# Kernel optimization log

Measured on AMD Instinct MI355X. Metric: run time of the kernel, lower is better.

The kernel has to match this reference:

```python
import jax, jax.numpy as jnp
import numpy as np

KS = 5               # kernel_size per spline dimension
K3 = KS ** 3         # 125 weight matrices per SplineConv
NS = [16384, 4096, 1024, 256, 64]  # nodes per hierarchy level
DEG = 8


def spline_basis(pseudo):
    """Degree-1 open B-spline basis for 3D pseudo-coords in [0,1].
    Returns basis [E,8] and weight indices [E,8] into the K3 weights."""
    v = pseudo * (KS - 1)
    bot = jnp.minimum(jnp.floor(v), KS - 2)
    frac = v - bot                                  # [E,3]
    bot = bot.astype(jnp.int32)
    bits = jnp.array([[(s >> d) & 1 for d in range(3)] for s in range(8)], jnp.int32)  # [8,3]
    f = frac[:, None, :]                            # [E,1,3]
    basis = jnp.prod(jnp.where(bits[None] == 1, f, 1.0 - f), axis=-1)   # [E,8]
    strides = jnp.array([1, KS, KS * KS], jnp.int32)
    widx = jnp.sum((bot[:, None, :] + bits[None]) * strides, axis=-1)   # [E,8]
    return basis, widx


def spline_conv(x, src, dst, basis, widx, W, root, bias, n):
    """out_j = (1/deg_j) * sum_{i->j} sum_s B_s(u_ij) x_i W_{k(s)} + x_j root + bias.
    Accumulate basis-weighted source features into per-(node, weight-index)
    buckets, then one dense einsum with the 125 kernel weights."""
    in_c = x.shape[1]
    contrib = basis[..., None] * x[src][:, None, :]          # [E,8,in]
    flat = (dst[:, None] * K3 + widx).reshape(-1)            # [E*8]
    acc = jnp.zeros((n * K3, in_c), x.dtype).at[flat].add(contrib.reshape(-1, in_c))
    out = jnp.einsum('nki,kio->no', acc.reshape(n, K3, in_c), W)
    deg = jnp.zeros((n,), x.dtype).at[dst].add(1.0)
    return out / jnp.maximum(deg, 1.0)[:, None] + x @ root + bias


def setup_inputs() -> dict:
    rng = np.random.default_rng(0)
    inp = {}
    inp['x'] = jnp.asarray(rng.standard_normal((NS[0], 1)), jnp.float32)
    for l in range(4):
        e = NS[l] * DEG
        inp[f'src{l}'] = jnp.asarray(rng.integers(0, NS[l], e), jnp.int32)
        inp[f'dst{l}'] = jnp.asarray(rng.integers(0, NS[l], e), jnp.int32)
        inp[f'pseudo{l}'] = jnp.asarray(rng.random((e, 3)), jnp.float32)
        cl = np.arange(NS[l]) % NS[l + 1]  # guarantees every voxel cluster non-empty
        rng.shuffle(cl)
        inp[f'cluster{l}'] = jnp.asarray(cl, jnp.int32)
    chans = [(1, 32), (32, 32), (32, 64), (64, 64), (64, 64), (64, 64), (64, 64), (64, 64)]
    names = ['1', '12', '2', '3', '4', '5', '6', '7']
    for nm, (ci, co) in zip(names, chans):
        inp[f'W{nm}'] = jnp.asarray(rng.standard_normal((K3, ci, co)) / np.sqrt(8.0 * ci), jnp.float32)
        inp[f'R{nm}'] = jnp.asarray(rng.standard_normal((ci, co)) / np.sqrt(ci), jnp.float32)
        inp[f'B{nm}'] = jnp.zeros((co,), jnp.float32)
    inp['fc1_w'] = jnp.asarray(rng.standard_normal((64, 64)) / 8.0, jnp.float32)
    inp['fc1_b'] = jnp.zeros((64,), jnp.float32)
    inp['fc2_w'] = jnp.asarray(rng.standard_normal((64, 10)) / 8.0, jnp.float32)
    inp['fc2_b'] = jnp.zeros((10,), jnp.float32)
    return inp


def reference(x, pseudo0, pseudo1, pseudo2, pseudo3,
              src0, dst0, src1, dst1, src2, dst2, src3, dst3,
              cluster0, cluster1, cluster2, cluster3,
              W1, R1, B1, W12, R12, B12, W2, R2, B2, W3, R3, B3,
              W4, R4, B4, W5, R5, B5, W6, R6, B6, W7, R7, B7,
              fc1_w, fc1_b, fc2_w, fc2_b):
    elu = jax.nn.elu
    # level 0
    b, wi = spline_basis(pseudo0)
    h = elu(spline_conv(x, src0, dst0, b, wi, W1, R1, B1, NS[0]))
    h = elu(spline_conv(h, src0, dst0, b, wi, W12, R12, B12, NS[0]))
    h = jax.ops.segment_max(h, cluster0, num_segments=NS[1])   # voxel max pool 1
    # level 1
    b, wi = spline_basis(pseudo1)
    h = elu(spline_conv(h, src1, dst1, b, wi, W2, R2, B2, NS[1]))
    h = elu(spline_conv(h, src1, dst1, b, wi, W3, R3, B3, NS[1]))
    h = jax.ops.segment_max(h, cluster1, num_segments=NS[2])   # voxel max pool 2
    # level 2
    b, wi = spline_basis(pseudo2)
    h = elu(spline_conv(h, src2, dst2, b, wi, W4, R4, B4, NS[2]))
    h = elu(spline_conv(h, src2, dst2, b, wi, W5, R5, B5, NS[2]))
    h = jax.ops.segment_max(h, cluster2, num_segments=NS[3])   # voxel max pool 3
    # level 3
    b, wi = spline_basis(pseudo3)
    h = elu(spline_conv(h, src3, dst3, b, wi, W6, R6, B6, NS[3]))
    h = elu(spline_conv(h, src3, dst3, b, wi, W7, R7, B7, NS[3]))
    h = jax.ops.segment_max(h, cluster3, num_segments=NS[4])   # voxel max pool 4
    # readout head (dropout is identity in eval mode)
    g = h.mean(0)[None, :]
    g = g @ fc1_w + fc1_b
    g = g @ fc2_w + fc2_b
    return jax.nn.log_softmax(g, axis=1)
```

## Files before the change

kernel.cpp:

```cpp
#include <hip/hip_runtime.h>
#include <hip/hip_bf16.h>

#define KS 5
#define K3 125

typedef __attribute__((ext_vector_type(8))) short short8;
typedef __attribute__((ext_vector_type(4))) float floatx4;

__device__ inline unsigned enc_f(float f) {
    int b = __float_as_int(f);
    return (b >= 0) ? ((unsigned)b | 0x80000000u) : ~((unsigned)b);
}

__device__ inline unsigned short f2bf(float f) {
    unsigned u = __float_as_uint(f);
    u += 0x7FFFu + ((u >> 16) & 1u);
    return (unsigned short)(u >> 16);
}
__device__ inline float bf2f(unsigned short h) {
    return __uint_as_float((unsigned)h << 16);
}
__device__ inline unsigned pack2bf(float a, float b) {
    return (unsigned)f2bf(a) | ((unsigned)f2bf(b) << 16);
}

__device__ inline void edge_basis(const float* __restrict__ pseudo, int e,
                                  float* bs, int* ks) {
    float fr[3];
    int bot[3];
#pragma unroll
    for (int d = 0; d < 3; ++d) {
        float v = pseudo[e * 3 + d] * (float)(KS - 1);
        float fl = fminf(floorf(v), (float)(KS - 2));
        fr[d] = v - fl;
        bot[d] = (int)fl;
    }
    const int strides[3] = {1, KS, KS * KS};
#pragma unroll
    for (int s = 0; s < 8; ++s) {
        float b = 1.f;
        int w = 0;
#pragma unroll
        for (int d = 0; d < 3; ++d) {
            int bit = (s >> d) & 1;
            b *= bit ? fr[d] : (1.f - fr[d]);
            w += (bot[d] + bit) * strides[d];
        }
        bs[s] = b;
        ks[s] = w;
    }
}

__device__ inline void edge_fracs(const float* __restrict__ pseudo, int e, float* bs) {
    float fr[3];
#pragma unroll
    for (int d = 0; d < 3; ++d) {
        float v = pseudo[e * 3 + d] * (float)(KS - 1);
        float fl = fminf(floorf(v), (float)(KS - 2));
        fr[d] = v - fl;
    }
#pragma unroll
    for (int s = 0; s < 8; ++s) {
        float b = 1.f;
#pragma unroll
        for (int d = 0; d < 3; ++d) b *= ((s >> d) & 1) ? fr[d] : (1.f - fr[d]);
        bs[s] = b;
    }
}

__device__ inline int edge_bucket(const float* __restrict__ pseudo, int e) {
    int kb = 0;
#pragma unroll
    for (int d = 0; d < 3; ++d) {
        float v = pseudo[e * 3 + d] * (float)(KS - 1);
        int fl = (int)fminf(floorf(v), (float)(KS - 2));
        kb += fl << (2 * d);
    }
    return kb;
}

__global__ __launch_bounds__(256) void pre1(
    const float* __restrict__ p0, const float* __restrict__ p1,
    const float* __restrict__ p2, const float* __restrict__ p3,
    const int* __restrict__ d0, const int* __restrict__ d1,
    const int* __restrict__ d2, const int* __restrict__ d3,
    const int* __restrict__ c0, const int* __restrict__ c1,
    const int* __restrict__ c2, const int* __restrict__ c3,
    const float* __restrict__ w12, const float* __restrict__ w2,
    const float* __restrict__ w3, const float* __restrict__ w4,
    const float* __restrict__ w5, const float* __restrict__ w6,
    const float* __restrict__ w7,
    int* __restrict__ hpart, int* __restrict__ degi,
    int* __restrict__ ccnt, int* __restrict__ clist,
    short* __restrict__ Wt) {
    __shared__ float wls[64 * 65];
    __shared__ int h[64];
    int b = blockIdx.x;
    int t = threadIdx.x;
    if (b >= 765) {
        int sl = b - 765;
        const float* srcp;
        int IC, OC, lgI, lgO, per;
        size_t obase;
        if (sl < 125) {
            IC = 32; OC = 32; lgI = 5; lgO = 5; per = 1024;
            srcp = w12 + (size_t)sl * 1024;
            obase = (size_t)sl * 1024;
        } else if (sl < 250) {
            int k = sl - 125;
            IC = 32; OC = 64; lgI = 5; lgO = 6; per = 2048;
            srcp = w2 + (size_t)k * 2048;
            obase = 128000 + (size_t)k * 2048;
        } else {
            int q = sl - 250;
            int ts = q / 125;
            int k = q - ts * 125;
            const float* Ws[5] = {w3, w4, w5, w6, w7};
            IC = 64; OC = 64; lgI = 6; lgO = 6; per = 4096;
            srcp = Ws[ts] + (size_t)k * 4096;
            obase = 384000 + (size_t)ts * 512000 + (size_t)k * 4096;
        }
        for (int r = t; r < per; r += 256) {
            int i = r >> lgO, o = r & (OC - 1);
            wls[i * (OC + 1) + o] = srcp[r];
        }
        __syncthreads();
        for (int j = t; j < per; j += 256) {
            int o = j >> lgI, i = j & (IC - 1);
            Wt[obase + j] = (short)f2bf(wls[i * (OC + 1) + o]);
        }
        return;
    }
    if (b >= 680) {
        int idx = (b - 680) * 256 + t;
        int j, cof, nof;
        const int* cl;
        if (idx < 16384)      { j = idx;         cl = c0; cof = 0;    nof = 0; }
        else if (idx < 20480) { j = idx - 16384; cl = c1; cof = 4096; nof = 16384; }
        else if (idx < 21504) { j = idx - 20480; cl = c2; cof = 5120; nof = 20480; }
        else if (idx < 21760) { j = idx - 21504; cl = c3; cof = 5376; nof = 21504; }
        else return;
        int c = cl[j];
        int slot = atomicAdd(&ccnt[cof + c], 1) & 3;
        clist[nof + c * 4 + slot] = j;
        return;
    }
    int l, lb, E, dof;
    const float* ps;
    const int* ds;
    if (b < 512)      { l = 0; lb = b;       ps = p0; ds = d0; E = 131072; dof = 0; }
    else if (b < 640) { l = 1; lb = b - 512; ps = p1; ds = d1; E = 32768;  dof = 16384; }
    else if (b < 672) { l = 2; lb = b - 640; ps = p2; ds = d2; E = 8192;   dof = 20480; }
    else              { l = 3; lb = b - 672; ps = p3; ds = d3; E = 2048;   dof = 21504; }
    if (t < 64) h[t] = 0;
    __syncthreads();
    int e = lb * 256 + t;
    if (e < E) {
        atomicAdd(&h[edge_bucket(ps, e)], 1);
        atomicAdd(&degi[dof + ds[e]], 1);
    }
    __syncthreads();
    if (t < 64) hpart[b * 64 + t] = h[t];
}

__global__ __launch_bounds__(1024) void pre2(const int* __restrict__ hpart,
                                             int* __restrict__ bbase,
                                             int* __restrict__ tileOf,
                                             int* __restrict__ pack,
                                             const int* __restrict__ degi,
                                             int* __restrict__ off,
                                             int* __restrict__ cur) {
    int b = blockIdx.x;
    int t = threadIdx.x;
    __shared__ int ls[1024];
    __shared__ int aux[192];
    if (b < 4) {
        const int Nv[4] = {16384, 4096, 1024, 256};
        const int DOFv[4] = {0, 16384, 20480, 21504};
        const int OFFv[4] = {0, 16385, 20482, 21507};
        int l = b;
        int n = Nv[l];
        const int* d = degi + DOFv[l];
        int* o = off + OFFv[l];
        int* c = cur + DOFv[l];
        int per = (n + 1023) >> 10;
        int beg = t * per;
        int end = (beg + per < n) ? beg + per : n;
        int s = 0;
        for (int j = beg; j < end; ++j) s += d[j];
        ls[t] = s;
        __syncthreads();
        for (int dd = 1; dd < 1024; dd <<= 1) {
            int v = (t >= dd) ? ls[t - dd] : 0;
            __syncthreads();
            ls[t] += v;
            __syncthreads();
        }
        int base = (t == 0) ? 0 : ls[t - 1];
        for (int j = beg; j < end; ++j) {
            o[j] = base;
            c[j] = base;
            base += d[j];
        }
        if (t == 1023) o[n] = ls[1023];
    } else {
        const int TBv[4] = {0, 2112, 2688, 2880};
        const int MTv[4] = {2112, 576, 192, 96};
        const int HBv[4] = {0, 512, 640, 672};
        const int NBv[4] = {512, 128, 32, 8};
        int l = b - 4;
        int tileBase = TBv[l];
        int hb = HBv[l], nb = NBv[l];
        int bucket = t & 63, seg = t >> 6;
        int rps = (nb + 15) >> 4;
        int r0 = seg * rps;
        int r1 = r0 + rps;
        if (r1 > nb) r1 = nb;
        int ssum = 0;
        for (int lb = r0; lb < r1; ++lb) ssum += hpart[(hb + lb) * 64 + bucket];
        ls[seg * 64 + bucket] = ssum;
        __syncthreads();
        int pre = 0;
        for (int s2 = 0; s2 < seg; ++s2) pre += ls[s2 * 64 + bucket];
        if (seg == 15) aux[bucket] = pre + ssum;
        __syncthreads();
        if (t < 64) aux[64 + t] = (aux[t] + 63) >> 6;
        __syncthreads();
        for (int d = 1; d < 64; d <<= 1) {
            int v = 0;
            if (t < 64 && t >= d) v = aux[64 + t - d];
            __syncthreads();
            if (t < 64) aux[64 + t] += v;
            __syncthreads();
        }
        if (t < 64) {
            int cnt = aux[t];
            int tiles = (cnt + 63) >> 6;
            int tb = tileBase + aux[64 + t] - tiles;
            int gstart = tb * 64;
            aux[128 + t] = gstart;
            for (int q = 0; q < tiles; ++q) tileOf[tb + q] = t;
            for (int idx = gstart + cnt; idx < (tb + tiles) * 64; ++idx) pack[idx] = -1;
            if (t == 63) {
                for (int q = tileBase + aux[64 + 63]; q < tileBase + MTv[l]; ++q)
                    tileOf[q] = -1;
            }
        }
        __syncthreads();
        int run = aux[128 + bucket] + pre;
        for (int lb = r0; lb < r1; ++lb) {
            bbase[(hb + lb) * 64 + bucket] = run;
            run += hpart[(hb + lb) * 64 + bucket];
        }
    }
}

__global__ __launch_bounds__(256) void scatter_pos_all(
    const float* __restrict__ p0, const float* __restrict__ p1,
    const float* __restrict__ p2, const float* __restrict__ p3,
    const int* __restrict__ d0, const int* __restrict__ d1,
    const int* __restrict__ d2, const int* __restrict__ d3,
    const int* __restrict__ bbase, int* __restrict__ cur,
    int* __restrict__ pack, int* __restrict__ posArr,
    int* __restrict__ esrt) {
    int b = blockIdx.x;
    int l, lb, E, dof, eof_;
    const float* ps;
    const int* ds;
    if (b < 512)      { l = 0; lb = b;       ps = p0; ds = d0; E = 131072; dof = 0;     eof_ = 0; }
    else if (b < 640) { l = 1; lb = b - 512; ps = p1; ds = d1; E = 32768;  dof = 16384; eof_ = 131072; }
    else if (b < 672) { l = 2; lb = b - 640; ps = p2; ds = d2; E = 8192;   dof = 20480; eof_ = 163840; }
    else              { l = 3; lb = b - 672; ps = p3; ds = d3; E = 2048;   dof = 21504; eof_ = 172032; }
    __shared__ int h[64], lbk[64], gb[64], sh[64];
    __shared__ int sp[256];
    __shared__ unsigned char skk[256];
    int t = threadIdx.x;
    int e = lb * 256 + t;
    int kb = -1;
    if (t < 64) {
        h[t] = 0;
        gb[t] = bbase[b * 64 + t];
    }
    __syncthreads();
    if (e < E) {
        kb = edge_bucket(ps, e);
        atomicAdd(&h[kb], 1);
        int p = atomicAdd(&cur[dof + ds[e]], 1);
        posArr[eof_ + e] = p;
        if (l == 0 && p >= 0 && p < 131072) esrt[p] = e;
    }
    __syncthreads();
    if (t < 64) sh[t] = h[t];
    __syncthreads();
    for (int d = 1; d < 64; d <<= 1) {
        int v = (t < 64 && t >= d) ? sh[t - d] : 0;
        __syncthreads();
        if (t < 64) sh[t] += v;
        __syncthreads();
    }
    if (t < 64) {
        lbk[t] = sh[t] - h[t];
        h[t] = 0;
    }
    __syncthreads();
    if (kb >= 0) {
        int ppos = lbk[kb] + atomicAdd(&h[kb], 1);
        sp[ppos] = e;
        skk[ppos] = (unsigned char)kb;
    }
    __syncthreads();
    int Pb = E - lb * 256;
    if (Pb > 256) Pb = 256;
    if (t < Pb) {
        int k = skk[t];
        pack[gb[k] + (t - lbk[k])] = sp[t];
    }
}

__global__ __launch_bounds__(256) void conv1_fin(
    const float* __restrict__ x, const int* __restrict__ src,
    const float* __restrict__ pseudo, const int* __restrict__ esrt,
    const int* __restrict__ off, const float* __restrict__ W,
    const float* __restrict__ R, const float* __restrict__ B,
    float* __restrict__ out, int n, int Emax) {
    const int lane = threadIdx.x & 63;
    const int wid = threadIdx.x >> 6;
    const int sub = lane >> 5;
    const int o = lane & 31;
    int j = (blockIdx.x * 4 + wid) * 2 + sub;
    if (j >= n) return;
    int b0 = off[j], b1 = off[j + 1];
    if (b0 < 0) b0 = 0;
    if (b1 > Emax) b1 = Emax;
    float acc = 0.f;
    for (int r = b0; r < b1; ++r) {
        int e = esrt[r];
        float bs[8];
        int ks[8];
        edge_basis(pseudo, e, bs, ks);
        float w = 0.f;
#pragma unroll
        for (int s = 0; s < 8; ++s) w = fmaf(bs[s], W[ks[s] * 32 + o], w);
        acc = fmaf(w, x[src[e]], acc);
    }
    float d = fmaxf((float)(b1 - b0), 1.f);
    float v = acc / d + x[j] * R[o] + B[o];
    out[(size_t)j * 32 + o] = (v > 0.f) ? v : expm1f(v);
}

template <int IN_C, int OUT_C>
__global__ __launch_bounds__(256, 6) void mfma_conv(
    const float* __restrict__ x, const int* __restrict__ src,
    const float* __restrict__ pseudo, const int* __restrict__ pack,
    const int* __restrict__ tileOf, const int* __restrict__ pos,
    const short* __restrict__ Wt, unsigned short* __restrict__ y, int tileBase,
    int Emax) {
    constexpr int PH = (IN_C == 64) ? 4 : 2;
    constexpr int SPP = 8 / PH;
    constexpr int KPH = SPP * IN_C;
    constexpr int KP = KPH + 8;
    constexpr int NT = OUT_C / 16;
    constexpr int IP = IN_C / 4;
    __shared__ short As[64 * KP];
    __shared__ int posL[64];
    const int tid = threadIdx.x;
    int t = tileBase + blockIdx.x;
    int kb = tileOf[t];
    if (kb < 0 || kb >= 64) return;
    kb = __builtin_amdgcn_readfirstlane(kb);
    const int kbase = (kb & 3) + 5 * ((kb >> 2) & 3) + 25 * ((kb >> 4) & 3);
    const int eLoc = tid >> 2, part = tid & 3;
    int e = pack[t * 64 + eLoc];
    if (e >= Emax) e = -1;
    float bs[8];
    float4 xq[IP / 4];
    if (e >= 0) edge_fracs(pseudo, e, bs);
    else {
#pragma unroll
        for (int s = 0; s < 8; ++s) bs[s] = 0.f;
    }
    if (part == 0) posL[eLoc] = (e >= 0) ? pos[e] : -1;
#pragma unroll
    for (int g = 0; g < IP / 4; ++g)
        xq[g] = (e >= 0)
                    ? *(const float4*)(x + (size_t)src[e] * IN_C + part * IP + g * 4)
                    : make_float4(0.f, 0.f, 0.f, 0.f);
    const int wave = tid >> 6, lane = tid & 63;
    const int quad = lane >> 4, lm = lane & 15;
    floatx4 acc[NT];
#pragma unroll
    for (int nt = 0; nt < NT; ++nt) acc[nt] = (floatx4){0.f, 0.f, 0.f, 0.f};
    const short* myrow = &As[(wave * 16 + lm) * KP];
#pragma unroll
    for (int ph = 0; ph < PH; ++ph) {
        if (ph) __syncthreads();
#pragma unroll
        for (int s2 = 0; s2 < SPP; ++s2) {
            const float b = bs[ph * SPP + s2];
            short* rowp = &As[eLoc * KP + s2 * IN_C + part * IP];
#pragma unroll
            for (int g = 0; g < IP / 4; ++g) {
                unsigned lo = pack2bf(b * xq[g].x, b * xq[g].y);
                unsigned hi = pack2bf(b * xq[g].z, b * xq[g].w);
                *(uint2*)(rowp + 4 * g) = make_uint2(lo, hi);
            }
        }
        __syncthreads();
#pragma unroll
        for (int kstep = 0; kstep < KPH / 32; ++kstep) {
            const int kg = kstep * 32;
            const int s2 = kg / IN_C;
            const int i0 = kg % IN_C;
            const int s = ph * SPP + s2;
            const int ks = kbase + (s & 1) + 5 * ((s >> 1) & 1) + 25 * ((s >> 2) & 1);
            short8 a = *(const short8*)&myrow[kg + quad * 8];
#pragma unroll
            for (int nt = 0; nt < NT; ++nt) {
                const short* bp =
                    Wt + ((size_t)ks * OUT_C + nt * 16 + lm) * IN_C + i0 + quad * 8;
                short8 bfr = *(const short8*)bp;
                acc[nt] = __builtin_amdgcn_mfma_f32_16x16x32_bf16(a, bfr, acc[nt], 0, 0, 0);
            }
        }
    }
#pragma unroll
    for (int nt = 0; nt < NT; ++nt) {
#pragma unroll
        for (int r = 0; r < 4; ++r) {
            int row = wave * 16 + quad * 4 + r;
            int p = posL[row];
            if (p >= 0 && p < Emax) y[(size_t)p * OUT_C + nt * 16 + lm] = f2bf(acc[nt][r]);
        }
    }
}

template <int OUT_C>
__device__ inline float csr_sum(const int* __restrict__ off,
                                const unsigned short* __restrict__ y, int j, int o,
                                float& dcount) {
    int b0 = off[j], b1 = off[j + 1];
    if (b0 < 0) b0 = 0;
    if (b1 < b0) b1 = b0;
    dcount = fmaxf((float)(b1 - b0), 1.f);
    float s0 = 0.f, s1 = 0.f, s2 = 0.f, s3 = 0.f;
    int r = b0;
    for (; r + 4 <= b1; r += 4) {
        s0 += bf2f(y[(size_t)(r + 0) * OUT_C + o]);
        s1 += bf2f(y[(size_t)(r + 1) * OUT_C + o]);
        s2 += bf2f(y[(size_t)(r + 2) * OUT_C + o]);
        s3 += bf2f(y[(size_t)(r + 3) * OUT_C + o]);
    }
    for (; r < b1; ++r) s0 += bf2f(y[(size_t)r * OUT_C + o]);
    return (s0 + s1) + (s2 + s3);
}

template <int IN_C, int OUT_C>
__global__ __launch_bounds__(256) void fin_gather_k(
    const float* __restrict__ xin, const float* __restrict__ R,
    const float* __restrict__ B, const int* __restrict__ off,
    const unsigned short* __restrict__ y, float* __restrict__ out, int n) {
    const int lane = threadIdx.x & 63;
    const int wid = threadIdx.x >> 6;
    constexpr int EPW = 64 / OUT_C;
    const int sub = (EPW == 2) ? (lane >> 5) : 0;
    const int o = lane & (OUT_C - 1);
    int j = (blockIdx.x * (blockDim.x >> 6) + wid) * EPW + sub;
    if (j >= n) return;
    float xv = (o < IN_C) ? xin[j * IN_C + o] : 0.f;
    float acc = B[o];
#pragma unroll 4
    for (int i = 0; i < IN_C; ++i) {
        float xi = __shfl(xv, i, OUT_C);
        acc = fmaf(xi, R[i * OUT_C + o], acc);
    }
    float d;
    float s = csr_sum<OUT_C>(off, y, j, o, d);
    float v = s / d + acc;
    out[j * OUT_C + o] = (v > 0.f) ? v : expm1f(v);
}

template <int IN_C, int OUT_C>
__global__ __launch_bounds__(256) void fin_pool_k(
    const float* __restrict__ xin, const float* __restrict__ R,
    const float* __restrict__ B, const int* __restrict__ off,
    const unsigned short* __restrict__ y, const int* __restrict__ clist,
    float* __restrict__ out, int nsrc) {
    constexpr int CPB = 256 / (4 * OUT_C);
    const int t = threadIdx.x;
    const int o = t & (OUT_C - 1);
    const int mem = (t / OUT_C) & 3;
    const int g = t / (4 * OUT_C);
    const int c = blockIdx.x * CPB + g;
    int j = clist[c * 4 + mem];
    if (j < 0) j = 0;
    if (j >= nsrc) j = nsrc - 1;
    float xv = (o < IN_C) ? xin[(size_t)j * IN_C + o] : 0.f;
    float acc = B[o];
#pragma unroll 4
    for (int i = 0; i < IN_C; ++i) {
        float xi = __shfl(xv, i, OUT_C);
        acc = fmaf(xi, R[i * OUT_C + o], acc);
    }
    float d;
    float s = csr_sum<OUT_C>(off, y, j, o, d);
    float v = s / d + acc;
    v = (v > 0.f) ? v : expm1f(v);
    __shared__ float sh[256];
    sh[t] = v;
    __syncthreads();
    if (mem == 0) {
        const float* base = &sh[g * 4 * OUT_C];
        float r01 = fmaxf(base[o], base[OUT_C + o]);
        float r23 = fmaxf(base[2 * OUT_C + o], base[3 * OUT_C + o]);
        out[(size_t)c * OUT_C + o] = fmaxf(r01, r23);
    }
}

__global__ __launch_bounds__(256) void conv1_fused(const float* __restrict__ x,
                                                   const int* __restrict__ src,
                                                   const int* __restrict__ dst,
                                                   const float* __restrict__ pseudo,
                                                   const float* __restrict__ W,
                                                   float* __restrict__ out, int E) {
    const int lane = threadIdx.x & 63;
    const int wid = threadIdx.x >> 6;
    const int sub = lane >> 5;
    const int o = lane & 31;
    int e = (blockIdx.x * 4 + wid) * 2 + sub;
    if (e >= E) return;
    float bs[8];
    int ks[8];
    edge_basis(pseudo, e, bs, ks);
    float acc = 0.f;
#pragma unroll
    for (int s = 0; s < 8; ++s) acc = fmaf(bs[s], W[ks[s] * 32 + o], acc);
    atomicAdd(&out[(size_t)dst[e] * 32 + o], acc * x[src[e]]);
}

template <int IN_C, int OUT_C>
__global__ __launch_bounds__(256) void conv_edges_inline(
    const float* __restrict__ x, const int* __restrict__ src,
    const int* __restrict__ dst, const float* __restrict__ pseudo,
    const float* __restrict__ W, float* __restrict__ out, int E) {
    const int lane = threadIdx.x & 63;
    const int wid = threadIdx.x >> 6;
    constexpr int EPW = 64 / OUT_C;
    const int sub = (EPW == 2) ? (lane >> 5) : 0;
    const int o = lane & (OUT_C - 1);
    long e = (long)(blockIdx.x * (blockDim.x >> 6) + wid) * EPW + sub;
    if (e >= E) return;
    float bs[8];
    int ks[8];
    edge_basis(pseudo, e, bs, ks);
    const int s_ = src[e];
    const int d_ = dst[e];
    float xv = (o < IN_C) ? x[s_ * IN_C + o] : 0.f;
    float acc = 0.f;
#pragma unroll
    for (int s = 0; s < 8; ++s) {
        const float b = bs[s];
        const float* Wk = W + (long)ks[s] * IN_C * OUT_C;
#pragma unroll 4
        for (int i = 0; i < IN_C; ++i) {
            float xi = __shfl(xv, i, OUT_C);
            acc = fmaf(b * xi, Wk[i * OUT_C + o], acc);
        }
    }
    atomicAdd(&out[(long)d_ * OUT_C + o], acc);
}

__global__ void deg_kernel(const int* __restrict__ dst, float* __restrict__ deg, int E) {
    int e = blockIdx.x * blockDim.x + threadIdx.x;
    if (e >= E) return;
    atomicAdd(&deg[dst[e]], 1.0f);
}

template <int IN_C, int OUT_C>
__global__ __launch_bounds__(256) void finalize_k(
    const float* __restrict__ xin, const float* __restrict__ R,
    const float* __restrict__ B, const float* __restrict__ deg,
    float* __restrict__ out, int n) {
    const int lane = threadIdx.x & 63;
    const int wid = threadIdx.x >> 6;
    constexpr int EPW = 64 / OUT_C;
    const int sub = (EPW == 2) ? (lane >> 5) : 0;
    const int o = lane & (OUT_C - 1);
    int j = (blockIdx.x * (blockDim.x >> 6) + wid) * EPW + sub;
    if (j >= n) return;
    float xv = (o < IN_C) ? xin[j * IN_C + o] : 0.f;
    float acc = B[o];
#pragma unroll 4
    for (int i = 0; i < IN_C; ++i) {
        float xi = __shfl(xv, i, OUT_C);
        acc = fmaf(xi, R[i * OUT_C + o], acc);
    }
    float d = fmaxf(deg[j], 1.f);
    float v = out[j * OUT_C + o] / d + acc;
    out[j * OUT_C + o] = (v > 0.f) ? v : expm1f(v);
}

__global__ void pool_scatter(const float* __restrict__ h, const int* __restrict__ cluster,
                             unsigned* __restrict__ pool, int n, int logC) {
    int idx = blockIdx.x * blockDim.x + threadIdx.x;
    if (idx >= (n << logC)) return;
    int j = idx >> logC;
    int c = idx & ((1 << logC) - 1);
    atomicMax(&pool[(cluster[j] << logC) + c], enc_f(h[idx]));
}

__global__ void pool_decode(const unsigned* __restrict__ pool, float* __restrict__ out, int total) {
    int idx = blockIdx.x * blockDim.x + threadIdx.x;
    if (idx >= total) return;
    unsigned u = pool[idx];
    int b = (u & 0x80000000u) ? (int)(u & 0x7FFFFFFFu) : (int)(~u);
    out[idx] = __int_as_float(b);
}

__global__ void head_kernel(const float* __restrict__ h, const float* __restrict__ fc1w,
                            const float* __restrict__ fc1b, const float* __restrict__ fc2w,
                            const float* __restrict__ fc2b, float* __restrict__ out) {
    __shared__ float m[64], t[64], u[10];
    int lane = threadIdx.x;
    float s = 0.f;
    for (int j = 0; j < 64; ++j) s += h[j * 64 + lane];
    m[lane] = s * (1.f / 64.f);
    __syncthreads();
    float a = fc1b[lane];
    for (int i = 0; i < 64; ++i) a = fmaf(m[i], fc1w[i * 64 + lane], a);
    t[lane] = a;
    __syncthreads();
    if (lane < 10) {
        float b = fc2b[lane];
        for (int i = 0; i < 64; ++i) b = fmaf(t[i], fc2w[i * 10 + lane], b);
        u[lane] = b;
    }
    __syncthreads();
    if (lane < 10) {
        float mx = u[0];
        for (int i = 1; i < 10; ++i) mx = fmaxf(mx, u[i]);
        float se = 0.f;
        for (int i = 0; i < 10; ++i) se += expf(u[i] - mx);
        out[lane] = u[lane] - mx - logf(se);
    }
}

static inline int cdiv(int a, int b) { return (a + b - 1) / b; }

extern "C" void kernel_launch(void* const* d_in, const int* in_sizes, int n_in,
                              void* d_out, int out_size, void* d_ws, size_t ws_size,
                              hipStream_t stream) {
    const float* x = (const float*)d_in[0];
    const int* src[4] = {(const int*)d_in[1], (const int*)d_in[5], (const int*)d_in[9], (const int*)d_in[13]};
    const int* dst[4] = {(const int*)d_in[2], (const int*)d_in[6], (const int*)d_in[10], (const int*)d_in[14]};
    const float* pseudo[4] = {(const float*)d_in[3], (const float*)d_in[7], (const float*)d_in[11], (const float*)d_in[15]};
    const int* cluster[4] = {(const int*)d_in[4], (const int*)d_in[8], (const int*)d_in[12], (const int*)d_in[16]};
    const float* Wp[8], *Rp[8], *Bp[8];
    for (int l = 0; l < 8; ++l) {
        Wp[l] = (const float*)d_in[17 + 3 * l];
        Rp[l] = (const float*)d_in[18 + 3 * l];
        Bp[l] = (const float*)d_in[19 + 3 * l];
    }
    const float* fc1w = (const float*)d_in[41];
    const float* fc1b = (const float*)d_in[42];
    const float* fc2w = (const float*)d_in[43];
    const float* fc2b = (const float*)d_in[44];
    float* outp = (float*)d_out;

    const int NS[5] = {16384, 4096, 1024, 256, 64};
    const int ES[4] = {16384 * 8, 4096 * 8, 1024 * 8, 256 * 8};
    const int MT[4] = {2048 + 64, 512 + 64, 128 + 64, 32 + 64};
    const int TB_[4] = {0, 2112, 2112 + 576, 2112 + 576 + 192};
    const int TOT_TILES = 2112 + 576 + 192 + 96;
    const int DTOT = 21760;
    const int OFF2[4] = {0, 16385, 20482, 21507};
    const int OFFTOT = 21764;
    const int EBASE[4] = {0, 131072, 163840, 172032};
    const int ETOT = 174080;
    const int NODE_OFF[4] = {0, 16384, 20480, 21504};
    const int CCTOT = 4096 + 1024 + 256 + 64;
    const int HTOT = 680;
    const int WT_OFF[7] = {0, 128000, 384000, 896000, 1408000, 1920000, 2432000};
    const int WT_TOT = 2944000;
    const int NSLICE = 875;

    char* w = (char*)d_ws;
    auto take = [&](size_t bytes) -> char* {
        char* r = w;
        w += (bytes + 255) & ~(size_t)255;
        return r;
    };
    float* bufA = (float*)take((size_t)NS[0] * 64 * 4);
    float* bufB = (float*)take((size_t)NS[0] * 64 * 4);
    unsigned* pool = (unsigned*)take((size_t)NS[1] * 64 * 4);
    char* zbase = w;
    int* ccnt = (int*)take((size_t)CCTOT * 4);
    int* degi = (int*)take((size_t)DTOT * 4);
    size_t zbytes = (size_t)(w - zbase);
    size_t fallbackNeed = (size_t)(w - (char*)d_ws);
    int* tileOf = (int*)take((size_t)TOT_TILES * 4);
    int* hpart = (int*)take((size_t)HTOT * 64 * 4);
    int* bbase = (int*)take((size_t)HTOT * 64 * 4);
    int* pack = (int*)take((size_t)TOT_TILES * 64 * 4);
    int* csr = (int*)take((size_t)OFFTOT * 4);
    int* cur = (int*)take((size_t)DTOT * 4);
    int* posArr = (int*)take((size_t)ETOT * 4);
    int* clist = (int*)take((size_t)DTOT * 4);
    int* esrt = (int*)take((size_t)ES[0] * 4);
    short* Wtb = (short*)take((size_t)WT_TOT * 2);
    unsigned short* y = (unsigned short*)take((size_t)ES[0] * 32 * 2);
    size_t need = (size_t)(w - (char*)d_ws);
    bool fast = ws_size >= need;

    const int TB = 256;

    if (fast) {
        (void)hipMemsetAsync(zbase, 0, zbytes, stream);
        pre1<<<765 + NSLICE, 256, 0, stream>>>(
            pseudo[0], pseudo[1], pseudo[2], pseudo[3],
            dst[0], dst[1], dst[2], dst[3],
            cluster[0], cluster[1], cluster[2], cluster[3],
            Wp[1], Wp[2], Wp[3], Wp[4], Wp[5], Wp[6], Wp[7],
            hpart, degi, ccnt, clist, Wtb);
        pre2<<<8, 1024, 0, stream>>>(hpart, bbase, tileOf, pack, degi, csr, cur);
        scatter_pos_all<<<680, 256, 0, stream>>>(pseudo[0], pseudo[1], pseudo[2], pseudo[3],
                                                 dst[0], dst[1], dst[2], dst[3],
                                                 bbase, cur, pack, posArr, esrt);

        {
            int n = NS[0];
            const int* off = csr + OFF2[0];
            const int* pos = posArr + EBASE[0];
            conv1_fin<<<cdiv(n, 8), TB, 0, stream>>>(x, src[0], pseudo[0], esrt, off,
                                                     Wp[0], Rp[0], Bp[0], bufA, n, ES[0]);
            mfma_conv<32, 32><<<MT[0], TB, 0, stream>>>(
                bufA, src[0], pseudo[0], pack, tileOf, pos, Wtb + WT_OFF[0], y, TB_[0], ES[0]);
            fin_pool_k<32, 32><<<NS[1] / 2, TB, 0, stream>>>(
                bufA, Rp[1], Bp[1], off, y, clist + NODE_OFF[0], bufB, NS[0]);
        }
        {
            int n = NS[1];
            const int* off = csr + OFF2[1];
            const int* pos = posArr + EBASE[1];
            mfma_conv<32, 64><<<MT[1], TB, 0, stream>>>(
                bufB, src[1], pseudo[1], pack, tileOf, pos, Wtb + WT_OFF[1], y, TB_[1], ES[1]);
            fin_gather_k<32, 64><<<cdiv(n, 4), TB, 0, stream>>>(bufB, Rp[2], Bp[2], off, y, bufA, n);
            mfma_conv<64, 64><<<MT[1], TB, 0, stream>>>(
                bufA, src[1], pseudo[1], pack, tileOf, pos, Wtb + WT_OFF[2], y, TB_[1], ES[1]);
            fin_pool_k<64, 64><<<NS[2], TB, 0, stream>>>(
                bufA, Rp[3], Bp[3], off, y, clist + NODE_OFF[1], bufB, NS[1]);
        }
        {
            int n = NS[2];
            const int* off = csr + OFF2[2];
            const int* pos = posArr + EBASE[2];
            mfma_conv<64, 64><<<MT[2], TB, 0, stream>>>(
                bufB, src[2], pseudo[2], pack, tileOf, pos, Wtb + WT_OFF[3], y, TB_[2], ES[2]);
            fin_gather_k<64, 64><<<cdiv(n, 4), TB, 0, stream>>>(bufB, Rp[4], Bp[4], off, y, bufA, n);
            mfma_conv<64, 64><<<MT[2], TB, 0, stream>>>(
                bufA, src[2], pseudo[2], pack, tileOf, pos, Wtb + WT_OFF[4], y, TB_[2], ES[2]);
            fin_pool_k<64, 64><<<NS[3], TB, 0, stream>>>(
                bufA, Rp[5], Bp[5], off, y, clist + NODE_OFF[2], bufB, NS[2]);
        }
        {
            int n = NS[3];
            const int* off = csr + OFF2[3];
            const int* pos = posArr + EBASE[3];
            mfma_conv<64, 64><<<MT[3], TB, 0, stream>>>(
                bufB, src[3], pseudo[3], pack, tileOf, pos, Wtb + WT_OFF[5], y, TB_[3], ES[3]);
            fin_gather_k<64, 64><<<cdiv(n, 4), TB, 0, stream>>>(bufB, Rp[6], Bp[6], off, y, bufA, n);
            mfma_conv<64, 64><<<MT[3], TB, 0, stream>>>(
                bufA, src[3], pseudo[3], pack, tileOf, pos, Wtb + WT_OFF[6], y, TB_[3], ES[3]);
            fin_pool_k<64, 64><<<NS[4], TB, 0, stream>>>(
                bufA, Rp[7], Bp[7], off, y, clist + NODE_OFF[3], bufB, NS[3]);
        }
        head_kernel<<<1, 64, 0, stream>>>(bufB, fc1w, fc1b, fc2w, fc2b, outp);
    } else if (ws_size >= fallbackNeed) {
        float* h0 = bufA;
        float* h1 = bufB;
        float* deg = (float*)degi;
        for (int l = 0; l < 4; ++l) {
            int E = ES[l], n = NS[l];
            (void)hipMemsetAsync(deg, 0, n * 4, stream);
            deg_kernel<<<cdiv(E, TB), TB, 0, stream>>>(dst[l], deg, E);
            for (int cc = 0; cc < 2; ++cc) {
                int li = (l == 0) ? cc : 2 * l + cc;
                if (l == 0 && cc == 0) {
                    (void)hipMemsetAsync(h0, 0, (size_t)n * 32 * 4, stream);
                    conv1_fused<<<cdiv(E, 8), TB, 0, stream>>>(x, src[0], dst[0], pseudo[0], Wp[0], h0, E);
                    finalize_k<1, 32><<<cdiv(n, 8), TB, 0, stream>>>(x, Rp[0], Bp[0], deg, h0, n);
                } else {
                    int ic = (l == 0) ? 32 : ((l == 1 && cc == 0) ? 32 : 64);
                    int oc = (l == 0) ? 32 : 64;
                    (void)hipMemsetAsync(h1, 0, (size_t)n * oc * 4, stream);
                    if (ic == 32 && oc == 32) {
                        conv_edges_inline<32, 32><<<cdiv(E, 8), TB, 0, stream>>>(h0, src[l], dst[l], pseudo[l], Wp[li], h1, E);
                        finalize_k<32, 32><<<cdiv(n, 8), TB, 0, stream>>>(h0, Rp[li], Bp[li], deg, h1, n);
                    } else if (ic == 32) {
                        conv_edges_inline<32, 64><<<cdiv(E, 4), TB, 0, stream>>>(h0, src[l], dst[l], pseudo[l], Wp[li], h1, E);
                        finalize_k<32, 64><<<cdiv(n, 4), TB, 0, stream>>>(h0, Rp[li], Bp[li], deg, h1, n);
                    } else {
                        conv_edges_inline<64, 64><<<cdiv(E, 4), TB, 0, stream>>>(h0, src[l], dst[l], pseudo[l], Wp[li], h1, E);
                        finalize_k<64, 64><<<cdiv(n, 4), TB, 0, stream>>>(h0, Rp[li], Bp[li], deg, h1, n);
                    }
                    float* tmp = h0; h0 = h1; h1 = tmp;
                }
            }
            int oc = (l == 0) ? 32 : 64;
            int logC = (l == 0) ? 5 : 6;
            (void)hipMemsetAsync(pool, 0, (size_t)NS[l + 1] * oc * 4, stream);
            pool_scatter<<<cdiv(n * oc, TB), TB, 0, stream>>>(h0, cluster[l], pool, n, logC);
            pool_decode<<<cdiv(NS[l + 1] * oc, TB), TB, 0, stream>>>(pool, h1, NS[l + 1] * oc);
            float* tmp = h0; h0 = h1; h1 = tmp;
        }
        head_kernel<<<1, 64, 0, stream>>>(h0, fc1w, fc1b, fc2w, fc2b, outp);
    }
}
```

Measured before the change: 403.0 us.

## Reuse degree-count atomics as CSR slot offsets and prefetch edges in conv1

The degree-counting atomic in pre1 now returns each edge's rank within its destination, which is saved into posArr. scatter_pos_all then computes the CSR position as offset plus rank, so the second round of atomics on a cur array goes away, along with cur's initialization in pre2. conv1_fin also prefetches the next edge's pseudo-coordinates and source feature, and computes the spline basis inline. This cuts atomic traffic and memory latency in the preprocessing and first-layer kernels, at the cost of an extra posArr write and read.

```diff
diff --git a/kernel.cpp b/kernel.cpp
--- a/kernel.cpp
+++ b/kernel.cpp
@@ -92,7 +92,7 @@
     const float* __restrict__ w7,
     int* __restrict__ hpart, int* __restrict__ degi,
     int* __restrict__ ccnt, int* __restrict__ clist,
-    short* __restrict__ Wt) {
+    short* __restrict__ Wt, int* __restrict__ posArr) {
     __shared__ float wls[64 * 65];
     __shared__ int h[64];
     int b = blockIdx.x;
@@ -145,19 +145,20 @@
         clist[nof + c * 4 + slot] = j;
         return;
     }
-    int l, lb, E, dof;
+    int l, lb, E, dof, eof_;
     const float* ps;
     const int* ds;
-    if (b < 512)      { l = 0; lb = b;       ps = p0; ds = d0; E = 131072; dof = 0; }
-    else if (b < 640) { l = 1; lb = b - 512; ps = p1; ds = d1; E = 32768;  dof = 16384; }
-    else if (b < 672) { l = 2; lb = b - 640; ps = p2; ds = d2; E = 8192;   dof = 20480; }
-    else              { l = 3; lb = b - 672; ps = p3; ds = d3; E = 2048;   dof = 21504; }
+    if (b < 512)      { l = 0; lb = b;       ps = p0; ds = d0; E = 131072; dof = 0;     eof_ = 0; }
+    else if (b < 640) { l = 1; lb = b - 512; ps = p1; ds = d1; E = 32768;  dof = 16384; eof_ = 131072; }
+    else if (b < 672) { l = 2; lb = b - 640; ps = p2; ds = d2; E = 8192;   dof = 20480; eof_ = 163840; }
+    else              { l = 3; lb = b - 672; ps = p3; ds = d3; E = 2048;   dof = 21504; eof_ = 172032; }
     if (t < 64) h[t] = 0;
     __syncthreads();
     int e = lb * 256 + t;
     if (e < E) {
         atomicAdd(&h[edge_bucket(ps, e)], 1);
-        atomicAdd(&degi[dof + ds[e]], 1);
+        int rel = atomicAdd(&degi[dof + ds[e]], 1);
+        posArr[eof_ + e] = rel;
     }
     __syncthreads();
     if (t < 64) hpart[b * 64 + t] = h[t];
@@ -168,8 +169,7 @@
                                              int* __restrict__ tileOf,
                                              int* __restrict__ pack,
                                              const int* __restrict__ degi,
-                                             int* __restrict__ off,
-                                             int* __restrict__ cur) {
+                                             int* __restrict__ off) {
     int b = blockIdx.x;
     int t = threadIdx.x;
     __shared__ int ls[1024];
@@ -182,7 +182,6 @@
         int n = Nv[l];
         const int* d = degi + DOFv[l];
         int* o = off + OFFv[l];
-        int* c = cur + DOFv[l];
         int per = (n + 1023) >> 10;
         int beg = t * per;
         int end = (beg + per < n) ? beg + per : n;
@@ -199,7 +198,6 @@
         int base = (t == 0) ? 0 : ls[t - 1];
         for (int j = beg; j < end; ++j) {
             o[j] = base;
-            c[j] = base;
             base += d[j];
         }
         if (t == 1023) o[n] = ls[1023];
@@ -260,17 +258,18 @@
     const float* __restrict__ p2, const float* __restrict__ p3,
     const int* __restrict__ d0, const int* __restrict__ d1,
     const int* __restrict__ d2, const int* __restrict__ d3,
-    const int* __restrict__ bbase, int* __restrict__ cur,
+    const int* __restrict__ bbase, const int* __restrict__ csr,
     int* __restrict__ pack, int* __restrict__ posArr,
     int* __restrict__ esrt) {
     int b = blockIdx.x;
-    int l, lb, E, dof, eof_;
+    int l, lb, E, eof_, cof;
     const float* ps;
     const int* ds;
-    if (b < 512)      { l = 0; lb = b;       ps = p0; ds = d0; E = 131072; dof = 0;     eof_ = 0; }
-    else if (b < 640) { l = 1; lb = b - 512; ps = p1; ds = d1; E = 32768;  dof = 16384; eof_ = 131072; }
-    else if (b < 672) { l = 2; lb = b - 640; ps = p2; ds = d2; E = 8192;   dof = 20480; eof_ = 163840; }
-    else              { l = 3; lb = b - 672; ps = p3; ds = d3; E = 2048;   dof = 21504; eof_ = 172032; }
+    if (b < 512)      { l = 0; lb = b;       ps = p0; ds = d0; E = 131072; eof_ = 0;      cof = 0; }
+    else if (b < 640) { l = 1; lb = b - 512; ps = p1; ds = d1; E = 32768;  eof_ = 131072; cof = 16385; }
+    else if (b < 672) { l = 2; lb = b - 640; ps = p2; ds = d2; E = 8192;   eof_ = 163840; cof = 20482; }
+    else              { l = 3; lb = b - 672; ps = p3; ds = d3; E = 2048;   eof_ = 172032; cof = 21507; }
+    const int* csrL = csr + cof;
     __shared__ int h[64], lbk[64], gb[64], sh[64];
     __shared__ int sp[256];
     __shared__ unsigned char skk[256];
@@ -285,7 +284,7 @@
     if (e < E) {
         kb = edge_bucket(ps, e);
         atomicAdd(&h[kb], 1);
-        int p = atomicAdd(&cur[dof + ds[e]], 1);
+        int p = csrL[ds[e]] + posArr[eof_ + e];
         posArr[eof_ + e] = p;
         if (l == 0 && p >= 0 && p < 131072) esrt[p] = e;
     }
@@ -333,15 +332,48 @@
     if (b0 < 0) b0 = 0;
     if (b1 > Emax) b1 = Emax;
     float acc = 0.f;
+    float px = 0.f, py = 0.f, pz = 0.f, xs = 0.f;
+    if (b0 < b1) {
+        int e0 = esrt[b0];
+        px = pseudo[e0 * 3];
+        py = pseudo[e0 * 3 + 1];
+        pz = pseudo[e0 * 3 + 2];
+        xs = x[src[e0]];
+    }
     for (int r = b0; r < b1; ++r) {
-        int e = esrt[r];
-        float bs[8];
-        int ks[8];
-        edge_basis(pseudo, e, bs, ks);
+        float cpx = px, cpy = py, cpz = pz, cxs = xs;
+        if (r + 1 < b1) {
+            int e1 = esrt[r + 1];
+            px = pseudo[e1 * 3];
+            py = pseudo[e1 * 3 + 1];
+            pz = pseudo[e1 * 3 + 2];
+            xs = x[src[e1]];
+        }
+        float fr[3];
+        int bot[3];
+        float pv[3] = {cpx, cpy, cpz};
+#pragma unroll
+        for (int d = 0; d < 3; ++d) {
+            float v = pv[d] * (float)(KS - 1);
+            float fl = fminf(floorf(v), (float)(KS - 2));
+            fr[d] = v - fl;
+            bot[d] = (int)fl;
+        }
+        const int strides[3] = {1, KS, KS * KS};
         float w = 0.f;
 #pragma unroll
-        for (int s = 0; s < 8; ++s) w = fmaf(bs[s], W[ks[s] * 32 + o], w);
-        acc = fmaf(w, x[src[e]], acc);
+        for (int s = 0; s < 8; ++s) {
+            float bsv = 1.f;
+            int wk = 0;
+#pragma unroll
+            for (int d = 0; d < 3; ++d) {
+                int bit = (s >> d) & 1;
+                bsv *= bit ? fr[d] : (1.f - fr[d]);
+                wk += (bot[d] + bit) * strides[d];
+            }
+            w = fmaf(bsv, W[wk * 32 + o], w);
+        }
+        acc = fmaf(w, cxs, acc);
     }
     float d = fmaxf((float)(b1 - b0), 1.f);
     float v = acc / d + x[j] * R[o] + B[o];
@@ -702,7 +734,6 @@
     int* bbase = (int*)take((size_t)HTOT * 64 * 4);
     int* pack = (int*)take((size_t)TOT_TILES * 64 * 4);
     int* csr = (int*)take((size_t)OFFTOT * 4);
-    int* cur = (int*)take((size_t)DTOT * 4);
     int* posArr = (int*)take((size_t)ETOT * 4);
     int* clist = (int*)take((size_t)DTOT * 4);
     int* esrt = (int*)take((size_t)ES[0] * 4);
@@ -720,11 +751,11 @@
             dst[0], dst[1], dst[2], dst[3],
             cluster[0], cluster[1], cluster[2], cluster[3],
             Wp[1], Wp[2], Wp[3], Wp[4], Wp[5], Wp[6], Wp[7],
-            hpart, degi, ccnt, clist, Wtb);
-        pre2<<<8, 1024, 0, stream>>>(hpart, bbase, tileOf, pack, degi, csr, cur);
+            hpart, degi, ccnt, clist, Wtb, posArr);
+        pre2<<<8, 1024, 0, stream>>>(hpart, bbase, tileOf, pack, degi, csr);
         scatter_pos_all<<<680, 256, 0, stream>>>(pseudo[0], pseudo[1], pseudo[2], pseudo[3],
                                                  dst[0], dst[1], dst[2], dst[3],
-                                                 bbase, cur, pack, posArr, esrt);
+                                                 bbase, csr, pack, posArr, esrt);
 
         {
             int n = NS[0];
```

Result: faster. 388.2 us (median of 2 runs) (-3.7%).
